# Kernel tuning notes

Measured on AMD Instinct MI355X. Metric: run time of the kernel, lower is better.

## Reference

```python
import jax, jax.numpy as jnp
import numpy as np

B, S, D, H = 128, 4096, 64, 256  # num_mlps, tokens per MLP, d_model, d_hidden


def setup_inputs() -> dict:
    key = jax.random.key(0)
    kx, k1, k2 = jax.random.split(key, 3)
    x = jax.random.normal(kx, (B, S, D), dtype=jnp.float32)
    # Stacked per-MLP weights (one 2-layer SiLU MLP per batch index, no bias)
    W1 = jax.random.normal(k1, (B, D, H), dtype=jnp.float32) * (1.0 / np.sqrt(D))
    W2 = jax.random.normal(k2, (B, H, D), dtype=jnp.float32) * (1.0 / np.sqrt(H))
    return {"x": x, "W1": W1, "W2": W2}


def reference(x, W1, W2):
    # outputs[i] = mlp_i(x[i]); stacked + residual -> one batched GEMM pair
    h = jax.nn.silu(jnp.einsum('bsd,bdh->bsh', x, W1))  # [B,S,H]
    out = jnp.einsum('bsh,bhd->bsd', h, W2)             # [B,S,D]
    return out + x
```

## Files before the change

kernel.cpp:

```cpp
#include <hip/hip_runtime.h>
#include <stdint.h>

#define BB 128
#define SS 4096
#define DD 64
#define HH 256

typedef short bf16x8 __attribute__((ext_vector_type(8)));
typedef float f32x16 __attribute__((ext_vector_type(16)));

__device__ __forceinline__ uint32_t cvt_pk_bf16(float lo, float hi) {
  uint32_t r;
  asm("v_cvt_pk_bf16_f32 %0, %1, %2" : "=v"(r) : "v"(lo), "v"(hi));
  return r;
}

__device__ __forceinline__ void permswap(uint32_t& a, uint32_t& b) {
  asm("v_permlane32_swap_b32 %0, %1" : "+v"(a), "+v"(b));
}

__device__ __forceinline__ float silu_f(float v) {
  float e = __expf(-v);
  return v * __builtin_amdgcn_rcpf(1.0f + e);
}

__device__ __forceinline__ void gload16(const void* g, void* l) {
  __builtin_amdgcn_global_load_lds(
      (const __attribute__((address_space(1))) void*)g,
      (__attribute__((address_space(3))) void*)l, 16, 0, 0);
}

__global__ __launch_bounds__(256) void transpose_w(
    const float* __restrict__ W1, const float* __restrict__ W2,
    ushort* __restrict__ W1t, ushort* __restrict__ W2t) {
  int g = blockIdx.x * 256 + threadIdx.x;
  const int half = (BB * DD * HH) / 8;
  float v[8];
  if (g < half) {
    size_t e = (size_t)g * 8;
    int b = (int)(e >> 14);
    int rem = (int)(e & 16383);
    int h = rem >> 6;
    int d0 = rem & 63;
    const float* src = W1 + ((size_t)b << 14) + h;
#pragma unroll
    for (int j = 0; j < 8; ++j) v[j] = src[(size_t)(d0 + j) << 8];
    uint4 o;
    o.x = cvt_pk_bf16(v[0], v[1]); o.y = cvt_pk_bf16(v[2], v[3]);
    o.z = cvt_pk_bf16(v[4], v[5]); o.w = cvt_pk_bf16(v[6], v[7]);
    *reinterpret_cast<uint4*>(W1t + e) = o;
  } else if (g < 2 * half) {
    size_t e = (size_t)(g - half) * 8;
    int b = (int)(e >> 14);
    int rem = (int)(e & 16383);
    int d = rem >> 8;
    int h0 = rem & 255;
    const float* src = W2 + ((size_t)b << 14) + d;
#pragma unroll
    for (int j = 0; j < 8; ++j) v[j] = src[(size_t)(h0 + j) << 6];
    uint4 o;
    o.x = cvt_pk_bf16(v[0], v[1]); o.y = cvt_pk_bf16(v[2], v[3]);
    o.z = cvt_pk_bf16(v[4], v[5]); o.w = cvt_pk_bf16(v[6], v[7]);
    *reinterpret_cast<uint4*>(W2t + e) = o;
  }
}

__global__ __launch_bounds__(512, 4) void mlp_fused(
    const float* __restrict__ xg, const ushort* __restrict__ w1t,
    const ushort* __restrict__ w2t, float* __restrict__ outg) {
  __shared__ int4 lds4[65536 / 16];
  char* lds = (char*)lds4;

  const int tid = threadIdx.x;
  const int wave = tid >> 6;
  const int lane = tid & 63;
  const int l31 = lane & 31;
  const int g5 = lane >> 5;

  int raw = blockIdx.x;
  int logical = (raw & 7) * 256 + (raw >> 3);
  const int b = logical >> 4;
  const int st = logical & 15;
  const int s_base = st * 256 + wave * 32;

  const float* xb = xg + (((size_t)b * SS + s_base) << 6);
  const ushort* w1b = w1t + ((size_t)b << 14);
  const ushort* w2b = w2t + ((size_t)b << 14);

#pragma unroll
  for (int r = 0; r < 4; ++r) {
    uint32_t o = (uint32_t)(r * 8192 + tid * 16);
    gload16((const char*)w1b + (o ^ (((o >> 7) & 7) << 4)), lds + o);
    gload16((const char*)w2b + (o ^ (((o >> 9) & 31) << 4)), lds + 32768 + o);
  }

  bf16x8 bx[4];
#pragma unroll
  for (int kc = 0; kc < 4; ++kc) {
    const float* p = xb + ((size_t)l31 << 6) + kc * 16 + g5 * 8;
    float4 fa = *reinterpret_cast<const float4*>(p);
    float4 fb = *reinterpret_cast<const float4*>(p + 4);
    union { uint32_t u[4]; bf16x8 v; } cv;
    cv.u[0] = cvt_pk_bf16(fa.x, fa.y);
    cv.u[1] = cvt_pk_bf16(fa.z, fa.w);
    cv.u[2] = cvt_pk_bf16(fb.x, fb.y);
    cv.u[3] = cvt_pk_bf16(fb.z, fb.w);
    bx[kc] = cv.v;
  }

  f32x16 acc[2];
  {
    const float* prow = xb + ((size_t)l31 << 6);
#pragma unroll
    for (int mt = 0; mt < 2; ++mt)
#pragma unroll
      for (int q = 0; q < 4; ++q) {
        float4 v =
            *reinterpret_cast<const float4*>(prow + mt * 32 + q * 8 + g5 * 4);
        acc[mt][4 * q + 0] = v.x;
        acc[mt][4 * q + 1] = v.y;
        acc[mt][4 * q + 2] = v.z;
        acc[mt][4 * q + 3] = v.w;
      }
  }

  __syncthreads();

  const f32x16 vzero = {0.f, 0.f, 0.f, 0.f, 0.f, 0.f, 0.f, 0.f,
                        0.f, 0.f, 0.f, 0.f, 0.f, 0.f, 0.f, 0.f};

#pragma unroll
  for (int hc = 0; hc < 8; ++hc) {
    bf16x8 a1[4];
#pragma unroll
    for (int kc = 0; kc < 4; ++kc) {
      uint32_t o = (uint32_t)((hc * 32 + l31) * 128 + kc * 32 + g5 * 16);
      o ^= ((o >> 7) & 7) << 4;
      a1[kc] = *reinterpret_cast<const bf16x8*>(lds + o);
    }
    f32x16 ah = vzero;
#pragma unroll
    for (int kc = 0; kc < 4; ++kc)
      ah = __builtin_amdgcn_mfma_f32_32x32x16_bf16(a1[kc], bx[kc], ah, 0, 0, 0);

    bf16x8 bh[2];
#pragma unroll
    for (int c = 0; c < 2; ++c) {
      uint32_t A0 = cvt_pk_bf16(silu_f(ah[8 * c + 0]), silu_f(ah[8 * c + 1]));
      uint32_t A1 = cvt_pk_bf16(silu_f(ah[8 * c + 2]), silu_f(ah[8 * c + 3]));
      uint32_t B0 = cvt_pk_bf16(silu_f(ah[8 * c + 4]), silu_f(ah[8 * c + 5]));
      uint32_t B1 = cvt_pk_bf16(silu_f(ah[8 * c + 6]), silu_f(ah[8 * c + 7]));
      permswap(A0, B0);
      permswap(A1, B1);
      union { uint32_t u[4]; bf16x8 v; } f;
      f.u[0] = A0; f.u[1] = A1; f.u[2] = B0; f.u[3] = B1;
      bh[c] = f.v;
    }

    bf16x8 a2[2][2];
#pragma unroll
    for (int mt = 0; mt < 2; ++mt)
#pragma unroll
      for (int c = 0; c < 2; ++c) {
        uint32_t o = (uint32_t)((mt * 32 + l31) * 512 + hc * 64 + c * 32 + g5 * 16);
        o ^= ((o >> 9) & 31) << 4;
        a2[mt][c] = *reinterpret_cast<const bf16x8*>(lds + 32768 + o);
      }
#pragma unroll
    for (int c = 0; c < 2; ++c)
#pragma unroll
      for (int mt = 0; mt < 2; ++mt)
        acc[mt] = __builtin_amdgcn_mfma_f32_32x32x16_bf16(a2[mt][c], bh[c],
                                                          acc[mt], 0, 0, 0);
  }

  float* prow = outg + (((size_t)b * SS + s_base + l31) << 6);
#pragma unroll
  for (int mt = 0; mt < 2; ++mt)
#pragma unroll
    for (int q = 0; q < 4; ++q) {
      float4 v;
      v.x = acc[mt][4 * q + 0];
      v.y = acc[mt][4 * q + 1];
      v.z = acc[mt][4 * q + 2];
      v.w = acc[mt][4 * q + 3];
      *reinterpret_cast<float4*>(prow + mt * 32 + q * 8 + g5 * 4) = v;
    }
}

extern "C" void kernel_launch(void* const* d_in, const int* in_sizes, int n_in,
                              void* d_out, int out_size, void* d_ws, size_t ws_size,
                              hipStream_t stream) {
  const float* x  = (const float*)d_in[0];
  const float* W1 = (const float*)d_in[1];
  const float* W2 = (const float*)d_in[2];
  float* out = (float*)d_out;

  ushort* W1t = (ushort*)d_ws;
  ushort* W2t = W1t + (size_t)BB * DD * HH;

  transpose_w<<<2048, 256, 0, stream>>>(W1, W2, W1t, W2t);
  mlp_fused<<<2048, 512, 0, stream>>>(x, W1t, W2t, out);
}
```

Before: 91.38 us.

## Pre-swizzle weights into MFMA fragment order and software-pipeline GEMM1 across hidden chunks

The weight prep kernel now writes W1 and W2 in bf16 directly in MFMA operand fragment order, so each lane reads a contiguous 16-byte slot at lane*16 plus a tile offset. This drops the XOR swizzle address math and gives conflict-free LDS reads. The main loop is also software-pipelined: the first-layer MFMAs for the next hidden chunk are issued before the second-layer MFMAs of the current chunk, so SiLU and MFMA latency can overlap. This keeps two f32x16 accumulators live, which raises register pressure at 4 waves/SIMD occupancy.

```diff
diff --git a/kernel.cpp b/kernel.cpp
--- a/kernel.cpp
+++ b/kernel.cpp
@@ -32,7 +32,7 @@
 
 __global__ __launch_bounds__(256) void transpose_w(
     const float* __restrict__ W1, const float* __restrict__ W2,
-    ushort* __restrict__ W1t, ushort* __restrict__ W2t) {
+    ushort* __restrict__ W1f, ushort* __restrict__ W2f) {
   int g = blockIdx.x * 256 + threadIdx.x;
   const int half = (BB * DD * HH) / 8;
   float v[8];
@@ -40,34 +40,40 @@
     size_t e = (size_t)g * 8;
     int b = (int)(e >> 14);
     int rem = (int)(e & 16383);
-    int h = rem >> 6;
-    int d0 = rem & 63;
+    int tile = rem >> 9;
+    int lane6 = (rem >> 3) & 63;
+    int hc = tile >> 2, kc = tile & 3;
+    int h = hc * 32 + (lane6 & 31);
+    int d0 = kc * 16 + (lane6 >> 5) * 8;
     const float* src = W1 + ((size_t)b << 14) + h;
 #pragma unroll
     for (int j = 0; j < 8; ++j) v[j] = src[(size_t)(d0 + j) << 8];
     uint4 o;
     o.x = cvt_pk_bf16(v[0], v[1]); o.y = cvt_pk_bf16(v[2], v[3]);
     o.z = cvt_pk_bf16(v[4], v[5]); o.w = cvt_pk_bf16(v[6], v[7]);
-    *reinterpret_cast<uint4*>(W1t + e) = o;
+    *reinterpret_cast<uint4*>(W1f + e) = o;
   } else if (g < 2 * half) {
     size_t e = (size_t)(g - half) * 8;
     int b = (int)(e >> 14);
     int rem = (int)(e & 16383);
-    int d = rem >> 8;
-    int h0 = rem & 255;
+    int tile = rem >> 9;
+    int lane6 = (rem >> 3) & 63;
+    int hc = tile >> 2, mt = (tile >> 1) & 1, c = tile & 1;
+    int d = mt * 32 + (lane6 & 31);
+    int h0 = hc * 32 + c * 16 + (lane6 >> 5) * 8;
     const float* src = W2 + ((size_t)b << 14) + d;
 #pragma unroll
     for (int j = 0; j < 8; ++j) v[j] = src[(size_t)(h0 + j) << 6];
     uint4 o;
     o.x = cvt_pk_bf16(v[0], v[1]); o.y = cvt_pk_bf16(v[2], v[3]);
     o.z = cvt_pk_bf16(v[4], v[5]); o.w = cvt_pk_bf16(v[6], v[7]);
-    *reinterpret_cast<uint4*>(W2t + e) = o;
+    *reinterpret_cast<uint4*>(W2f + e) = o;
   }
 }
 
 __global__ __launch_bounds__(512, 4) void mlp_fused(
-    const float* __restrict__ xg, const ushort* __restrict__ w1t,
-    const ushort* __restrict__ w2t, float* __restrict__ outg) {
+    const float* __restrict__ xg, const ushort* __restrict__ w1f,
+    const ushort* __restrict__ w2f, float* __restrict__ outg) {
   __shared__ int4 lds4[65536 / 16];
   char* lds = (char*)lds4;
 
@@ -84,14 +90,14 @@
   const int s_base = st * 256 + wave * 32;
 
   const float* xb = xg + (((size_t)b * SS + s_base) << 6);
-  const ushort* w1b = w1t + ((size_t)b << 14);
-  const ushort* w2b = w2t + ((size_t)b << 14);
+  const char* w1b = (const char*)(w1f + ((size_t)b << 14));
+  const char* w2b = (const char*)(w2f + ((size_t)b << 14));
 
 #pragma unroll
   for (int r = 0; r < 4; ++r) {
     uint32_t o = (uint32_t)(r * 8192 + tid * 16);
-    gload16((const char*)w1b + (o ^ (((o >> 7) & 7) << 4)), lds + o);
-    gload16((const char*)w2b + (o ^ (((o >> 9) & 31) << 4)), lds + 32768 + o);
+    gload16(w1b + o, lds + o);
+    gload16(w2b + o, lds + 32768 + o);
   }
 
   bf16x8 bx[4];
@@ -126,30 +132,28 @@
 
   __syncthreads();
 
+  const char* lw1 = lds + lane * 16;
+  const char* lw2 = lds + 32768 + lane * 16;
+
   const f32x16 vzero = {0.f, 0.f, 0.f, 0.f, 0.f, 0.f, 0.f, 0.f,
                         0.f, 0.f, 0.f, 0.f, 0.f, 0.f, 0.f, 0.f};
 
+  f32x16 ah_cur = vzero;
+#pragma unroll
+  for (int kc = 0; kc < 4; ++kc) {
+    bf16x8 a1 = *reinterpret_cast<const bf16x8*>(lw1 + kc * 1024);
+    ah_cur = __builtin_amdgcn_mfma_f32_32x32x16_bf16(a1, bx[kc], ah_cur, 0, 0, 0);
+  }
+
 #pragma unroll
   for (int hc = 0; hc < 8; ++hc) {
-    bf16x8 a1[4];
-#pragma unroll
-    for (int kc = 0; kc < 4; ++kc) {
-      uint32_t o = (uint32_t)((hc * 32 + l31) * 128 + kc * 32 + g5 * 16);
-      o ^= ((o >> 7) & 7) << 4;
-      a1[kc] = *reinterpret_cast<const bf16x8*>(lds + o);
-    }
-    f32x16 ah = vzero;
-#pragma unroll
-    for (int kc = 0; kc < 4; ++kc)
-      ah = __builtin_amdgcn_mfma_f32_32x32x16_bf16(a1[kc], bx[kc], ah, 0, 0, 0);
-
     bf16x8 bh[2];
 #pragma unroll
     for (int c = 0; c < 2; ++c) {
-      uint32_t A0 = cvt_pk_bf16(silu_f(ah[8 * c + 0]), silu_f(ah[8 * c + 1]));
-      uint32_t A1 = cvt_pk_bf16(silu_f(ah[8 * c + 2]), silu_f(ah[8 * c + 3]));
-      uint32_t B0 = cvt_pk_bf16(silu_f(ah[8 * c + 4]), silu_f(ah[8 * c + 5]));
-      uint32_t B1 = cvt_pk_bf16(silu_f(ah[8 * c + 6]), silu_f(ah[8 * c + 7]));
+      uint32_t A0 = cvt_pk_bf16(silu_f(ah_cur[8 * c + 0]), silu_f(ah_cur[8 * c + 1]));
+      uint32_t A1 = cvt_pk_bf16(silu_f(ah_cur[8 * c + 2]), silu_f(ah_cur[8 * c + 3]));
+      uint32_t B0 = cvt_pk_bf16(silu_f(ah_cur[8 * c + 4]), silu_f(ah_cur[8 * c + 5]));
+      uint32_t B1 = cvt_pk_bf16(silu_f(ah_cur[8 * c + 6]), silu_f(ah_cur[8 * c + 7]));
       permswap(A0, B0);
       permswap(A1, B1);
       union { uint32_t u[4]; bf16x8 v; } f;
@@ -157,21 +161,28 @@
       bh[c] = f.v;
     }
 
-    bf16x8 a2[2][2];
-#pragma unroll
-    for (int mt = 0; mt < 2; ++mt)
-#pragma unroll
-      for (int c = 0; c < 2; ++c) {
-        uint32_t o = (uint32_t)((mt * 32 + l31) * 512 + hc * 64 + c * 32 + g5 * 16);
-        o ^= ((o >> 9) & 31) << 4;
-        a2[mt][c] = *reinterpret_cast<const bf16x8*>(lds + 32768 + o);
+    f32x16 ah_nxt = vzero;
+    if (hc < 7) {
+#pragma unroll
+      for (int kc = 0; kc < 4; ++kc) {
+        bf16x8 a1 = *reinterpret_cast<const bf16x8*>(
+            lw1 + ((hc + 1) * 4 + kc) * 1024);
+        ah_nxt =
+            __builtin_amdgcn_mfma_f32_32x32x16_bf16(a1, bx[kc], ah_nxt, 0, 0, 0);
       }
+    }
+
 #pragma unroll
     for (int c = 0; c < 2; ++c)
 #pragma unroll
-      for (int mt = 0; mt < 2; ++mt)
-        acc[mt] = __builtin_amdgcn_mfma_f32_32x32x16_bf16(a2[mt][c], bh[c],
-                                                          acc[mt], 0, 0, 0);
+      for (int mt = 0; mt < 2; ++mt) {
+        bf16x8 a2 = *reinterpret_cast<const bf16x8*>(
+            lw2 + (hc * 4 + mt * 2 + c) * 1024);
+        acc[mt] =
+            __builtin_amdgcn_mfma_f32_32x32x16_bf16(a2, bh[c], acc[mt], 0, 0, 0);
+      }
+
+    ah_cur = ah_nxt;
   }
 
   float* prow = outg + (((size_t)b * SS + s_base + l31) << 6);
@@ -196,9 +207,9 @@
   const float* W2 = (const float*)d_in[2];
   float* out = (float*)d_out;
 
-  ushort* W1t = (ushort*)d_ws;
-  ushort* W2t = W1t + (size_t)BB * DD * HH;
-
-  transpose_w<<<2048, 256, 0, stream>>>(W1, W2, W1t, W2t);
-  mlp_fused<<<2048, 512, 0, stream>>>(x, W1t, W2t, out);
-}
+  ushort* W1f = (ushort*)d_ws;
+  ushort* W2f = W1f + (size_t)BB * DD * HH;
+
+  transpose_w<<<2048, 256, 0, stream>>>(W1, W2, W1f, W2f);
+  mlp_fused<<<2048, 512, 0, stream>>>(x, W1f, W2f, out);
+}
```

Result: faster. 86.93 us (-4.9%).
